# Optimization experiments

Measured on AMD Instinct MI355X. Metric: run time of the kernel, lower is better.

The kernel has to match this reference:

```python
import jax, jax.numpy as jnp
import numpy as np

EPS = 1e-12  # matches F.normalize default eps

def _angle(e):
    # e: [N, D] embeddings
    d = e[:, None, :] - e[None, :, :]                      # [N, N, D] pairwise differences
    n = jnp.linalg.norm(d, axis=-1, keepdims=True)         # [N, N, 1]
    d = d / jnp.maximum(n, EPS)                            # normalized diffs; diagonal stays 0
    # all-triplet cosines: for each anchor i, Gram matrix of its normalized diffs
    return jnp.einsum('ijd,ikd->ijk', d, d)                # [N, N, N]

def _smooth_l1_mean(a, b):
    # torch F.smooth_l1_loss with beta=1.0, reduction='mean'
    x = jnp.abs(a - b)
    return jnp.mean(jnp.where(x < 1.0, 0.5 * x * x, x - 0.5))

def setup_inputs() -> dict:
    key = jax.random.key(0)
    k1, k2 = jax.random.split(key)
    student = jax.random.normal(k1, (384, 256), dtype=jnp.float32)
    teacher = jax.random.normal(k2, (384, 256), dtype=jnp.float32)
    return {"student": student, "teacher": teacher}

def reference(student, teacher):
    s_angle = _angle(student)
    t_angle = _angle(teacher)
    return _smooth_l1_mean(s_angle, t_angle)
```

## Files before the change

### kernel.cpp

```cpp
#include <hip/hip_runtime.h>

#define NPTS 384
#define DIMS 256
#define TI 4
#define JC 24

__global__ __launch_bounds__(64) void gram_kernel(const float* __restrict__ Es,
                                                  const float* __restrict__ Et,
                                                  float* __restrict__ Gs,
                                                  float* __restrict__ Gt) {
    const float* __restrict__ E = (blockIdx.z == 0) ? Es : Et;
    float* __restrict__ G       = (blockIdx.z == 0) ? Gs : Gt;

    __shared__ float AsT[32][36];
    __shared__ float BsT[32][36];

    const int t  = threadIdx.x;
    const int tx = t & 7;
    const int ty = t >> 3;
    const int i0 = blockIdx.x * 32;
    const int j0 = blockIdx.y * 32;

    float acc[4][4] = {};

    for (int k0 = 0; k0 < DIMS; k0 += 32) {
#pragma unroll
        for (int m = 0; m < 4; m++) {
            const int row = ty + 8 * m;
            float va[4], vb[4];
            *(float4*)va = *(const float4*)&E[(i0 + row) * DIMS + k0 + 4 * tx];
            *(float4*)vb = *(const float4*)&E[(j0 + row) * DIMS + k0 + 4 * tx];
#pragma unroll
            for (int q = 0; q < 4; q++) {
                AsT[4 * tx + q][row] = va[q];
                BsT[4 * tx + q][row] = vb[q];
            }
        }
        __syncthreads();
#pragma unroll
        for (int k = 0; k < 32; k++) {
            float a[4], b[4];
            *(float4*)a = *(const float4*)&AsT[k][4 * ty];
            *(float4*)b = *(const float4*)&BsT[k][4 * tx];
#pragma unroll
            for (int p = 0; p < 4; p++)
#pragma unroll
                for (int q = 0; q < 4; q++)
                    acc[p][q] = fmaf(a[p], b[q], acc[p][q]);
        }
        __syncthreads();
    }

#pragma unroll
    for (int p = 0; p < 4; p++) {
        float4 v = make_float4(acc[p][0], acc[p][1], acc[p][2], acc[p][3]);
        *(float4*)&G[(i0 + 4 * ty + p) * NPTS + j0 + 4 * tx] = v;
    }
}

__global__ void pack_kernel(const float* __restrict__ Gs, const float* __restrict__ Gt,
                            float4* __restrict__ P, float2* __restrict__ W) {
    int idx = blockIdx.x * 256 + threadIdx.x;
    if (idx >= NPTS * NPTS) return;
    int i = idx / NPTS;
    int j = idx - i * NPTS;

    float gs   = Gs[idx];
    float gt   = Gt[idx];
    float gsii = Gs[i * (NPTS + 1)];
    float gsjj = Gs[j * (NPTS + 1)];
    float gtii = Gt[i * (NPTS + 1)];
    float gtjj = Gt[j * (NPTS + 1)];

    float vs = fmaxf(gsii - 2.0f * gs + gsjj, 0.0f);
    float vt = fmaxf(gtii - 2.0f * gt + gtjj, 0.0f);
    float rs = (i == j) ? 0.0f : 1.0f / fmaxf(sqrtf(vs), 1e-12f);
    float rt = (i == j) ? 0.0f : 1.0f / fmaxf(sqrtf(vt), 1e-12f);

    P[idx] = make_float4(gsii - gs, rs, gtii - gt, rt);
    W[idx] = make_float2(gs, gt);
}

__global__ __launch_bounds__(NPTS) void rkd_angle_kernel(
        const float4* __restrict__ P, const float2* __restrict__ W,
        float* __restrict__ out) {
    const int k  = threadIdx.x;
    const int i0 = blockIdx.x * TI;
    const int j0 = blockIdx.y * JC;

    float rsk[TI], rtk[TI], nqs[TI], nqt[TI];
#pragma unroll
    for (int r = 0; r < TI; r++) {
        float4 pk = P[(i0 + r) * NPTS + k];
        float2 wk = W[(i0 + r) * NPTS + k];
        rsk[r] = pk.y;
        rtk[r] = pk.w;
        nqs[r] = -(pk.y * wk.x);
        nqt[r] = -(pk.w * wk.y);
    }

    float acc = 0.0f;
#pragma unroll 4
    for (int j = j0; j < j0 + JC; j++) {
        float2 w = W[j * NPTS + k];
#pragma unroll
        for (int r = 0; r < TI; r++) {
            float4 pj = P[(i0 + r) * NPTS + j];
            float as = pj.y * fmaf(rsk[r], w.x + pj.x, nqs[r]);
            float at = pj.w * fmaf(rtk[r], w.y + pj.z, nqt[r]);
            float d  = as - at;
            float ad = fabsf(d);
            float m  = fminf(ad, 1.0f);
            acc = fmaf(m, fmaf(-0.5f, m, ad), acc);
        }
    }

#pragma unroll
    for (int off = 32; off > 0; off >>= 1)
        acc += __shfl_down(acc, off, 64);

    __shared__ float wsum[NPTS / 64];
    const int wid  = k >> 6;
    const int lane = k & 63;
    if (lane == 0) wsum[wid] = acc;
    __syncthreads();
    if (k == 0) {
        float s = 0.0f;
#pragma unroll
        for (int w = 0; w < NPTS / 64; w++) s += wsum[w];
        atomicAdd(out, s * (1.0f / (384.0f * 384.0f * 384.0f)));
    }
}

extern "C" void kernel_launch(void* const* d_in, const int* in_sizes, int n_in,
                              void* d_out, int out_size, void* d_ws, size_t ws_size,
                              hipStream_t stream) {
    const float* student = (const float*)d_in[0];
    const float* teacher = (const float*)d_in[1];
    float* out = (float*)d_out;

    float4* P  = (float4*)d_ws;
    float2* W  = (float2*)(P + NPTS * NPTS);
    float*  Gs = (float*)(W + NPTS * NPTS);
    float*  Gt = Gs + NPTS * NPTS;

    hipMemsetAsync(d_out, 0, sizeof(float), stream);

    dim3 ggrid(NPTS / 32, NPTS / 32, 2);
    gram_kernel<<<ggrid, 64, 0, stream>>>(student, teacher, Gs, Gt);

    dim3 pgrid((NPTS * NPTS + 255) / 256, 1, 1);
    pack_kernel<<<pgrid, 256, 0, stream>>>(Gs, Gt, P, W);

    dim3 mgrid(NPTS / TI, NPTS / JC, 1);
    rkd_angle_kernel<<<mgrid, NPTS, 0, stream>>>(P, W, out);
}
```

Measured before the change: 101.8 us.

## Fuse pack into gram kernel, split P/W per tensor, widen anchor tile

Merges the pack step into the Gram GEMM epilogue. Squared norms are computed from the shared-memory tiles, and the packed P/W arrays are written directly, which removes the separate pack kernel, the intermediate G round trip and the memset launch. The output is now zeroed inside the gram kernel instead of by the memset. The P/W layout is split into separate student and teacher arrays. The angle kernel tile grows from 4 to 6 anchors with less unrolling. The extra diagonal-sum work in the GEMM loop and higher register pressure in the main kernel are the costs.

```diff
diff --git a/kernel.cpp b/kernel.cpp
--- a/kernel.cpp
+++ b/kernel.cpp
@@ -2,24 +2,35 @@
 
 #define NPTS 384
 #define DIMS 256
-#define TI 4
+#define TI 6
 #define JC 24
 
-__global__ __launch_bounds__(64) void gram_kernel(const float* __restrict__ Es,
-                                                  const float* __restrict__ Et,
-                                                  float* __restrict__ Gs,
-                                                  float* __restrict__ Gt) {
+__global__ __launch_bounds__(64) void gram_pack_kernel(
+        const float* __restrict__ Es, const float* __restrict__ Et,
+        float2* __restrict__ Ps, float2* __restrict__ Pt,
+        float* __restrict__ Ws, float* __restrict__ Wt,
+        float* __restrict__ out) {
     const float* __restrict__ E = (blockIdx.z == 0) ? Es : Et;
-    float* __restrict__ G       = (blockIdx.z == 0) ? Gs : Gt;
+    float2* __restrict__ P      = (blockIdx.z == 0) ? Ps : Pt;
+    float* __restrict__ W       = (blockIdx.z == 0) ? Ws : Wt;
+
+    if (blockIdx.x == 0 && blockIdx.y == 0 && blockIdx.z == 0 && threadIdx.x == 0)
+        out[0] = 0.0f;
 
     __shared__ float AsT[32][36];
     __shared__ float BsT[32][36];
+    __shared__ float dA[32];
+    __shared__ float dB[32];
 
     const int t  = threadIdx.x;
     const int tx = t & 7;
     const int ty = t >> 3;
     const int i0 = blockIdx.x * 32;
     const int j0 = blockIdx.y * 32;
+
+    const int e = t & 31;
+    const float* dsrc = (t < 32) ? &AsT[0][e] : &BsT[0][e];
+    float dsum = 0.0f;
 
     float acc[4][4] = {};
 
@@ -48,41 +59,42 @@
                 for (int q = 0; q < 4; q++)
                     acc[p][q] = fmaf(a[p], b[q], acc[p][q]);
         }
+#pragma unroll
+        for (int k = 0; k < 32; k++) {
+            float v = dsrc[k * 36];
+            dsum = fmaf(v, v, dsum);
+        }
         __syncthreads();
     }
 
+    if (t < 32) dA[e] = dsum; else dB[e] = dsum;
+    __syncthreads();
+
 #pragma unroll
     for (int p = 0; p < 4; p++) {
-        float4 v = make_float4(acc[p][0], acc[p][1], acc[p][2], acc[p][3]);
-        *(float4*)&G[(i0 + 4 * ty + p) * NPTS + j0 + 4 * tx] = v;
+        const int i   = i0 + 4 * ty + p;
+        const float dAv = dA[4 * ty + p];
+        float2 prow[4];
+        float  wrow[4];
+#pragma unroll
+        for (int q = 0; q < 4; q++) {
+            const int j   = j0 + 4 * tx + q;
+            const float g   = acc[p][q];
+            const float dBv = dB[4 * tx + q];
+            float v = fmaxf(dAv - 2.0f * g + dBv, 0.0f);
+            float r = (i == j) ? 0.0f : 1.0f / fmaxf(sqrtf(v), 1e-12f);
+            prow[q] = make_float2(dAv - g, r);
+            wrow[q] = g;
+        }
+        *(float4*)&P[i * NPTS + j0 + 4 * tx]     = make_float4(prow[0].x, prow[0].y, prow[1].x, prow[1].y);
+        *(float4*)&P[i * NPTS + j0 + 4 * tx + 2] = make_float4(prow[2].x, prow[2].y, prow[3].x, prow[3].y);
+        *(float4*)&W[i * NPTS + j0 + 4 * tx]     = make_float4(wrow[0], wrow[1], wrow[2], wrow[3]);
     }
 }
 
-__global__ void pack_kernel(const float* __restrict__ Gs, const float* __restrict__ Gt,
-                            float4* __restrict__ P, float2* __restrict__ W) {
-    int idx = blockIdx.x * 256 + threadIdx.x;
-    if (idx >= NPTS * NPTS) return;
-    int i = idx / NPTS;
-    int j = idx - i * NPTS;
-
-    float gs   = Gs[idx];
-    float gt   = Gt[idx];
-    float gsii = Gs[i * (NPTS + 1)];
-    float gsjj = Gs[j * (NPTS + 1)];
-    float gtii = Gt[i * (NPTS + 1)];
-    float gtjj = Gt[j * (NPTS + 1)];
-
-    float vs = fmaxf(gsii - 2.0f * gs + gsjj, 0.0f);
-    float vt = fmaxf(gtii - 2.0f * gt + gtjj, 0.0f);
-    float rs = (i == j) ? 0.0f : 1.0f / fmaxf(sqrtf(vs), 1e-12f);
-    float rt = (i == j) ? 0.0f : 1.0f / fmaxf(sqrtf(vt), 1e-12f);
-
-    P[idx] = make_float4(gsii - gs, rs, gtii - gt, rt);
-    W[idx] = make_float2(gs, gt);
-}
-
 __global__ __launch_bounds__(NPTS) void rkd_angle_kernel(
-        const float4* __restrict__ P, const float2* __restrict__ W,
+        const float2* __restrict__ Ps, const float2* __restrict__ Pt,
+        const float* __restrict__ Ws, const float* __restrict__ Wt,
         float* __restrict__ out) {
     const int k  = threadIdx.x;
     const int i0 = blockIdx.x * TI;
@@ -91,23 +103,27 @@
     float rsk[TI], rtk[TI], nqs[TI], nqt[TI];
 #pragma unroll
     for (int r = 0; r < TI; r++) {
-        float4 pk = P[(i0 + r) * NPTS + k];
-        float2 wk = W[(i0 + r) * NPTS + k];
-        rsk[r] = pk.y;
-        rtk[r] = pk.w;
-        nqs[r] = -(pk.y * wk.x);
-        nqt[r] = -(pk.w * wk.y);
+        float2 ps = Ps[(i0 + r) * NPTS + k];
+        float2 pt = Pt[(i0 + r) * NPTS + k];
+        float  ws = Ws[(i0 + r) * NPTS + k];
+        float  wt = Wt[(i0 + r) * NPTS + k];
+        rsk[r] = ps.y;
+        rtk[r] = pt.y;
+        nqs[r] = -(ps.y * ws);
+        nqt[r] = -(pt.y * wt);
     }
 
     float acc = 0.0f;
-#pragma unroll 4
+#pragma unroll 2
     for (int j = j0; j < j0 + JC; j++) {
-        float2 w = W[j * NPTS + k];
+        float ws = Ws[j * NPTS + k];
+        float wt = Wt[j * NPTS + k];
 #pragma unroll
         for (int r = 0; r < TI; r++) {
-            float4 pj = P[(i0 + r) * NPTS + j];
-            float as = pj.y * fmaf(rsk[r], w.x + pj.x, nqs[r]);
-            float at = pj.w * fmaf(rtk[r], w.y + pj.z, nqt[r]);
+            float2 pjs = Ps[(i0 + r) * NPTS + j];
+            float2 pjt = Pt[(i0 + r) * NPTS + j];
+            float as = pjs.y * fmaf(rsk[r], ws + pjs.x, nqs[r]);
+            float at = pjt.y * fmaf(rtk[r], wt + pjt.x, nqt[r]);
             float d  = as - at;
             float ad = fabsf(d);
             float m  = fminf(ad, 1.0f);
@@ -139,19 +155,14 @@
     const float* teacher = (const float*)d_in[1];
     float* out = (float*)d_out;
 
-    float4* P  = (float4*)d_ws;
-    float2* W  = (float2*)(P + NPTS * NPTS);
-    float*  Gs = (float*)(W + NPTS * NPTS);
-    float*  Gt = Gs + NPTS * NPTS;
-
-    hipMemsetAsync(d_out, 0, sizeof(float), stream);
+    float2* Ps = (float2*)d_ws;
+    float2* Pt = Ps + NPTS * NPTS;
+    float*  Ws = (float*)(Pt + NPTS * NPTS);
+    float*  Wt = Ws + NPTS * NPTS;
 
     dim3 ggrid(NPTS / 32, NPTS / 32, 2);
-    gram_kernel<<<ggrid, 64, 0, stream>>>(student, teacher, Gs, Gt);
-
-    dim3 pgrid((NPTS * NPTS + 255) / 256, 1, 1);
-    pack_kernel<<<pgrid, 256, 0, stream>>>(Gs, Gt, P, W);
+    gram_pack_kernel<<<ggrid, 64, 0, stream>>>(student, teacher, Ps, Pt, Ws, Wt, out);
 
     dim3 mgrid(NPTS / TI, NPTS / JC, 1);
-    rkd_angle_kernel<<<mgrid, NPTS, 0, stream>>>(P, W, out);
+    rkd_angle_kernel<<<mgrid, NPTS, 0, stream>>>(Ps, Pt, Ws, Wt, out);
 }
```

Measured after the change: 93.17 us. 8.5% less time.
